# Kernel optimization log

Hardware: AMD Instinct MI355X
Metric: run time of the kernel (lower is better)

Reference implementation:

```python
import jax, jax.numpy as jnp
import numpy as np

E = 16          # num experts
D_IN = 1024     # input_size
D_OUT = 4096    # output_size
TOKENS_PER_EXPERT = 2048
TOTAL_TOKENS = E * TOKENS_PER_EXPERT


def setup_inputs() -> dict:
    key = jax.random.key(0)
    k1, k2 = jax.random.split(key)
    inputs = jax.random.normal(k1, (TOTAL_TOKENS, D_IN), dtype=jnp.float32)
    # init matches nn.init.uniform_(-1/input_size, 1/input_size)
    weight = jax.random.uniform(k2, (E, D_IN, D_OUT), dtype=jnp.float32,
                                minval=-1.0 / D_IN, maxval=1.0 / D_IN)
    # per-expert token counts; host-side numpy constant (like expert_size.tolist() in torch)
    expert_size = np.full((E,), TOKENS_PER_EXPERT, dtype=np.int64)
    return {"inputs": inputs, "expert_size": expert_size, "weight": weight}


def grouped_mm(inputs, weight, sizes):
    # sizes: python ints (static). Each contiguous chunk of tokens hits its expert's weight.
    offs = np.concatenate([[0], np.cumsum(sizes)])
    outs = [inputs[offs[i]:offs[i + 1]] @ weight[i] for i in range(len(sizes))]
    return jnp.concatenate(outs, axis=0)  # [total_tokens, D_OUT]


def reference(inputs, expert_size, weight):
    sizes = np.asarray(expert_size).tolist()  # static split sizes, as in torch.split
    return grouped_mm(inputs, weight, sizes)
```

## Files before the change

### kernel.cpp

```cpp
#include <hip/hip_runtime.h>
#include <hip/hip_bf16.h>


#define E_NUM 16
#define M_PER_E 2048
#define K_DIM 1024
#define N_DIM 4096

#define A_ELEMS (E_NUM * M_PER_E * K_DIM)
#define W_ELEMS (E_NUM * K_DIM * N_DIM)
#define WS_NEEDED ((size_t)A_ELEMS * 2 + (size_t)W_ELEMS * 2)

typedef float  float4v  __attribute__((ext_vector_type(4)));
typedef float  f32x4    __attribute__((ext_vector_type(4)));
typedef short  bf16x8   __attribute__((ext_vector_type(8)));
typedef unsigned short ushort4v __attribute__((ext_vector_type(4)));
typedef unsigned short ushort8v __attribute__((ext_vector_type(8)));

__device__ __forceinline__ ushort4v cvt4_bf16(float4v f) {
    union { __bf16 h[4]; ushort4v u; } x;
#pragma unroll
    for (int j = 0; j < 4; ++j) x.h[j] = (__bf16)f[j];
    return x.u;
}

__global__ __launch_bounds__(256) void convertA_kernel(
    const float* __restrict__ A, unsigned short* __restrict__ out, int n8)
{
    int idx = blockIdx.x * 256 + threadIdx.x;
    int stride = gridDim.x * 256;
    for (int i = idx; i < n8; i += stride) {
        float4v a = *reinterpret_cast<const float4v*>(A + (size_t)i * 8);
        float4v b = *reinterpret_cast<const float4v*>(A + (size_t)i * 8 + 4);
        ushort8v v;
        ushort4v va = cvt4_bf16(a), vb = cvt4_bf16(b);
#pragma unroll
        for (int j = 0; j < 4; ++j) { v[j] = va[j]; v[j + 4] = vb[j]; }
        *reinterpret_cast<ushort8v*>(out + (size_t)i * 8) = v;
    }
}

__global__ __launch_bounds__(256) void transposeW_kernel(
    const float* __restrict__ W, unsigned short* __restrict__ WT)
{
    const int nt = blockIdx.x;
    const int kt = blockIdx.y;
    const int e  = blockIdx.z;
    const int t  = threadIdx.x;

    __shared__ __align__(16) float T[64 * 64];

    const float* Wb = W + ((size_t)e * K_DIM + (size_t)kt * 64) * N_DIM + nt * 64;

#pragma unroll
    for (int j = 0; j < 4; ++j) {
        int kl = (t >> 4) + j * 16;
        int n4 = t & 15;
        float4v v = *reinterpret_cast<const float4v*>(Wb + (size_t)kl * N_DIM + n4 * 4);
        int sp = n4 ^ ((kl >> 3) & 7);
        *reinterpret_cast<float4v*>(&T[kl * 64 + sp * 4]) = v;
    }
    __syncthreads();

#pragma unroll
    for (int c = 0; c < 2; ++c) {
        int nl = (t >> 3) + c * 32;
        int kc = t & 7;
        ushort8v v;
#pragma unroll
        for (int j = 0; j < 8; ++j) {
            int kl = kc * 8 + j;
            int sp = (nl >> 2) ^ kc;
            float f = T[kl * 64 + sp * 4 + (nl & 3)];
            union { __bf16 h; unsigned short u; } cv; cv.h = (__bf16)f;
            v[j] = cv.u;
        }
        unsigned short* dst = WT + ((size_t)e * N_DIM + (size_t)nt * 64 + nl) * K_DIM
                              + (size_t)kt * 64 + kc * 8;
        *reinterpret_cast<ushort8v*>(dst) = v;
    }
}

#define GBM 256
#define GBN 256
#define GBK 64
#define GKT (K_DIM / GBK)

__global__ __launch_bounds__(512, 2) void gemm_bf16_kernel(
    const unsigned short* __restrict__ A,
    const unsigned short* __restrict__ B,
    float* __restrict__ C)
{
    const int bid = blockIdx.x;
    const int swzid = (bid & 7) * (2048 / 8) + (bid >> 3);
    const int e   = swzid >> 7;
    const int rem = swzid & 127;
    const int bm  = rem >> 4;
    const int bn  = rem & 15;

    const int tid  = threadIdx.x;
    const int lane = tid & 63;
    const int wid  = tid >> 6;
    const int wm   = wid >> 2;
    const int wn   = wid & 3;
    const int lrow = lane & 15;
    const int kq   = lane >> 4;

    __shared__ __align__(16) unsigned short sA[2][GBM * GBK];
    __shared__ __align__(16) unsigned short sB[2][GBN * GBK];

    const unsigned short* Abase = A + ((size_t)e * M_PER_E + (size_t)bm * GBM) * K_DIM;
    const unsigned short* Bbase = B + ((size_t)e * N_DIM  + (size_t)bn * GBN) * K_DIM;
    float*                Cbase = C + ((size_t)e * M_PER_E + (size_t)bm * GBM) * N_DIM
                                    + (size_t)bn * GBN;

    const int schunk = (lane & 7) ^ ((lane >> 3) & 7);
    const int srow   = lane >> 3;

    auto STAGE = [&](int p, int kt) {
        const unsigned short* ak = Abase + (size_t)kt * GBK + schunk * 8;
        const unsigned short* bk = Bbase + (size_t)kt * GBK + schunk * 8;
#pragma unroll
        for (int i = 0; i < 4; ++i) {
            const int rb = i * 64 + wid * 8;
            __builtin_amdgcn_global_load_lds(
                (const __attribute__((address_space(1))) void*)(ak + (size_t)(rb + srow) * K_DIM),
                (__attribute__((address_space(3))) void*)&sA[p][rb * GBK], 16, 0, 0);
            __builtin_amdgcn_global_load_lds(
                (const __attribute__((address_space(1))) void*)(bk + (size_t)(rb + srow) * K_DIM),
                (__attribute__((address_space(3))) void*)&sB[p][rb * GBK], 16, 0, 0);
        }
    };

    f32x4 acc[8][4];
#pragma unroll
    for (int mf = 0; mf < 8; ++mf)
#pragma unroll
        for (int nf = 0; nf < 4; ++nf) acc[mf][nf] = (f32x4)0.0f;

    bf16x8 af[8][2], bf[4][2];

    auto READ_ALL = [&](int p) {
#pragma unroll
        for (int s = 0; s < 2; ++s) {
            const int slot = (s * 4 + kq) ^ (lrow & 7);
#pragma unroll
            for (int mf = 0; mf < 4; ++mf) {
                int row = wm * 128 + mf * 16 + lrow;
                af[mf][s] = *reinterpret_cast<const bf16x8*>(&sA[p][row * GBK + slot * 8]);
            }
#pragma unroll
            for (int nf = 0; nf < 4; ++nf) {
                int row = wn * 64 + nf * 16 + lrow;
                bf[nf][s] = *reinterpret_cast<const bf16x8*>(&sB[p][row * GBK + slot * 8]);
            }
        }
#pragma unroll
        for (int s = 0; s < 2; ++s) {
            const int slot = (s * 4 + kq) ^ (lrow & 7);
#pragma unroll
            for (int mf = 4; mf < 8; ++mf) {
                int row = wm * 128 + mf * 16 + lrow;
                af[mf][s] = *reinterpret_cast<const bf16x8*>(&sA[p][row * GBK + slot * 8]);
            }
        }
    };

    auto MMQ = [&](int mh, int nh) {
        __builtin_amdgcn_s_setprio(1);
#pragma unroll
        for (int s = 0; s < 2; ++s)
#pragma unroll
            for (int nf = nh * 2; nf < nh * 2 + 2; ++nf)
#pragma unroll
                for (int mf = mh * 4; mf < mh * 4 + 4; ++mf)
                    acc[mf][nf] = __builtin_amdgcn_mfma_f32_16x16x32_bf16(
                        af[mf][s], bf[nf][s], acc[mf][nf], 0, 0, 0);
        __builtin_amdgcn_s_setprio(0);
    };

    STAGE(0, 0);
    STAGE(1, 1);
    asm volatile("s_waitcnt vmcnt(8)" ::: "memory");
    __builtin_amdgcn_s_barrier();

#pragma unroll 1
    for (int t = 0; t < GKT; ++t) {
        const int p = t & 1;
        READ_ALL(p);
        MMQ(0, 0); MMQ(0, 1);
        asm volatile("s_waitcnt lgkmcnt(0)" ::: "memory");
        __builtin_amdgcn_s_barrier();
        if (t < GKT - 2) STAGE(p, t + 2);
        MMQ(1, 0); MMQ(1, 1);
        if (t < GKT - 1) {
            if (t < GKT - 2)
                asm volatile("s_waitcnt vmcnt(8)" ::: "memory");
            else
                asm volatile("s_waitcnt vmcnt(0)" ::: "memory");
            __builtin_amdgcn_s_barrier();
        }
    }

#pragma unroll
    for (int mf = 0; mf < 8; ++mf) {
#pragma unroll
        for (int nf = 0; nf < 4; ++nf) {
#pragma unroll
            for (int j = 0; j < 4; ++j) {
                int row = wm * 128 + mf * 16 + kq * 4 + j;
                int col = wn * 64 + nf * 16 + lrow;
                Cbase[(size_t)row * N_DIM + col] = acc[mf][nf][j];
            }
        }
    }
}

#define BM 128
#define BN 128
#define BK 64
#define KT (K_DIM / BK)

__device__ __forceinline__ int swz_f(int row, int kelem) {
    return kelem ^ (((row ^ (row >> 3)) & 7) << 3);
}

__global__ __launch_bounds__(256) void grouped_gemm_fused_kernel(
    const float* __restrict__ A, const float* __restrict__ W, float* __restrict__ C)
{
    const int bn = blockIdx.x;
    const int bm = blockIdx.y;
    const int e  = blockIdx.z;
    const int tid  = threadIdx.x;
    const int lane = tid & 63;
    const int wid  = tid >> 6;
    const int wr   = wid >> 1;
    const int wc   = wid & 1;

    __shared__ __align__(16) unsigned short fA[BM * BK];
    __shared__ __align__(16) unsigned short fB[BN * BK];

    const float* Abase = A + ((size_t)e * M_PER_E + (size_t)bm * BM) * K_DIM;
    const float* Wbase = W + (size_t)e * K_DIM * N_DIM + (size_t)bn * BN;
    float*       Cbase = C + ((size_t)e * M_PER_E + (size_t)bm * BM) * N_DIM + (size_t)bn * BN;

    const int arow  = tid >> 4;
    const int acol4 = (tid & 15) * 4;
    const int bkq   = tid >> 4;
    const int bnq   = tid & 15;

    f32x4 acc[4][4];
#pragma unroll
    for (int m = 0; m < 4; ++m)
#pragma unroll
        for (int n = 0; n < 4; ++n) acc[m][n] = (f32x4)0.0f;

    float4v ra[8], rb[8];

    auto LOADT = [&](int kt) {
        const float* ap = Abase + (size_t)arow * K_DIM + kt * BK + acol4;
#pragma unroll
        for (int i = 0; i < 8; ++i)
            ra[i] = *reinterpret_cast<const float4v*>(ap + (size_t)i * 16 * K_DIM);
        const float* bp = Wbase + (size_t)(kt * BK + bkq * 4) * N_DIM + bnq * 4;
#pragma unroll
        for (int i = 0; i < 2; ++i)
#pragma unroll
            for (int r = 0; r < 4; ++r)
                rb[i * 4 + r] = *reinterpret_cast<const float4v*>(bp + (size_t)r * N_DIM + i * 64);
    };

    auto STORET = [&]() {
#pragma unroll
        for (int i = 0; i < 8; ++i) {
            int row = arow + i * 16;
            ushort4v v = cvt4_bf16(ra[i]);
            *reinterpret_cast<ushort4v*>(&fA[row * BK + swz_f(row, acol4)]) = v;
        }
#pragma unroll
        for (int i = 0; i < 2; ++i) {
#pragma unroll
            for (int j = 0; j < 4; ++j) {
                int n = (bnq + i * 16) * 4 + j;
                float4v col;
                col[0] = rb[i * 4 + 0][j];
                col[1] = rb[i * 4 + 1][j];
                col[2] = rb[i * 4 + 2][j];
                col[3] = rb[i * 4 + 3][j];
                ushort4v v = cvt4_bf16(col);
                *reinterpret_cast<ushort4v*>(&fB[n * BK + swz_f(n, bkq * 4)]) = v;
            }
        }
    };

    auto COMPUTE = [&]() {
#pragma unroll
        for (int s = 0; s < 2; ++s) {
            bf16x8 af[4], bfr[4];
            const int ke = s * 32 + (lane >> 4) * 8;
#pragma unroll
            for (int m = 0; m < 4; ++m) {
                int row = wr * 64 + m * 16 + (lane & 15);
                af[m] = *reinterpret_cast<const bf16x8*>(&fA[row * BK + swz_f(row, ke)]);
            }
#pragma unroll
            for (int n = 0; n < 4; ++n) {
                int row = wc * 64 + n * 16 + (lane & 15);
                bfr[n] = *reinterpret_cast<const bf16x8*>(&fB[row * BK + swz_f(row, ke)]);
            }
#pragma unroll
            for (int m = 0; m < 4; ++m)
#pragma unroll
                for (int n = 0; n < 4; ++n)
                    acc[m][n] = __builtin_amdgcn_mfma_f32_16x16x32_bf16(
                        af[m], bfr[n], acc[m][n], 0, 0, 0);
        }
    };

    LOADT(0);
    STORET();
    __syncthreads();
    for (int kt = 0; kt < KT; ++kt) {
        if (kt + 1 < KT) LOADT(kt + 1);
        COMPUTE();
        __syncthreads();
        if (kt + 1 < KT) STORET();
        __syncthreads();
    }

#pragma unroll
    for (int m = 0; m < 4; ++m)
#pragma unroll
        for (int n = 0; n < 4; ++n)
#pragma unroll
            for (int j = 0; j < 4; ++j) {
                int row = wr * 64 + m * 16 + (lane >> 4) * 4 + j;
                int col = wc * 64 + n * 16 + (lane & 15);
                Cbase[(size_t)row * N_DIM + col] = acc[m][n][j];
            }
}

extern "C" void kernel_launch(void* const* d_in, const int* in_sizes, int n_in,
                              void* d_out, int out_size, void* d_ws, size_t ws_size,
                              hipStream_t stream) {
    const float* A = (const float*)d_in[0];
    const float* W = (const float*)d_in[2];
    float* out = (float*)d_out;

    if (ws_size >= WS_NEEDED) {
        unsigned short* wsA = (unsigned short*)d_ws;
        unsigned short* wsW = wsA + (size_t)A_ELEMS;

        hipLaunchKernelGGL(convertA_kernel, dim3(2048), dim3(256), 0, stream,
                           A, wsA, A_ELEMS / 8);
        hipLaunchKernelGGL(transposeW_kernel, dim3(N_DIM / 64, K_DIM / 64, E_NUM),
                           dim3(256), 0, stream, W, wsW);
        hipLaunchKernelGGL(gemm_bf16_kernel, dim3(2048), dim3(512), 0, stream,
                           wsA, wsW, out);
    } else {
        dim3 grid(N_DIM / BN, M_PER_E / BM, E_NUM);
        hipLaunchKernelGGL(grouped_gemm_fused_kernel, grid, dim3(256), 0, stream,
                           A, W, out);
    }
}
```

Before: 470.3 us.

## Interleave half-tile global-to-LDS staging with quarter MFMA phases in GEMM loop

Result: no change. 463.3 us, median of 2 (-1.5%).

```diff
diff --git a/kernel.cpp b/kernel.cpp
--- a/kernel.cpp
+++ b/kernel.cpp
@@ -85,6 +85,9 @@
 #define GBN 256
 #define GBK 64
 #define GKT (K_DIM / GBK)
+
+#define BAR()   __builtin_amdgcn_s_barrier()
+#define LGKM0() asm volatile("s_waitcnt lgkmcnt(0)" ::: "memory")
 
 __global__ __launch_bounds__(512, 2) void gemm_bf16_kernel(
     const unsigned short* __restrict__ A,
@@ -117,18 +120,24 @@
     const int schunk = (lane & 7) ^ ((lane >> 3) & 7);
     const int srow   = lane >> 3;
 
-    auto STAGE = [&](int p, int kt) {
-        const unsigned short* ak = Abase + (size_t)kt * GBK + schunk * 8;
-        const unsigned short* bk = Bbase + (size_t)kt * GBK + schunk * 8;
-#pragma unroll
-        for (int i = 0; i < 4; ++i) {
-            const int rb = i * 64 + wid * 8;
+    auto STAGE_A = [&](int t, int h) {
+        const unsigned short* g = Abase + (size_t)t * GBK + schunk * 8;
+#pragma unroll
+        for (int j = 0; j < 2; ++j) {
+            const int rb = h * 128 + (wid * 2 + j) * 8;
             __builtin_amdgcn_global_load_lds(
-                (const __attribute__((address_space(1))) void*)(ak + (size_t)(rb + srow) * K_DIM),
-                (__attribute__((address_space(3))) void*)&sA[p][rb * GBK], 16, 0, 0);
+                (const __attribute__((address_space(1))) void*)(g + (size_t)(rb + srow) * K_DIM),
+                (__attribute__((address_space(3))) void*)&sA[t & 1][rb * GBK], 16, 0, 0);
+        }
+    };
+    auto STAGE_B = [&](int t, int h) {
+        const unsigned short* g = Bbase + (size_t)t * GBK + schunk * 8;
+#pragma unroll
+        for (int j = 0; j < 2; ++j) {
+            const int rb = h * 128 + (wid * 2 + j) * 8;
             __builtin_amdgcn_global_load_lds(
-                (const __attribute__((address_space(1))) void*)(bk + (size_t)(rb + srow) * K_DIM),
-                (__attribute__((address_space(3))) void*)&sB[p][rb * GBK], 16, 0, 0);
+                (const __attribute__((address_space(1))) void*)(g + (size_t)(rb + srow) * K_DIM),
+                (__attribute__((address_space(3))) void*)&sB[t & 1][rb * GBK], 16, 0, 0);
         }
     };
 
@@ -138,30 +147,28 @@
 #pragma unroll
         for (int nf = 0; nf < 4; ++nf) acc[mf][nf] = (f32x4)0.0f;
 
-    bf16x8 af[8][2], bf[4][2];
-
-    auto READ_ALL = [&](int p) {
+    bf16x8 af[4][2];
+    bf16x8 bf[4][2];
+
+    auto READ_A = [&](int p, int mh) {
 #pragma unroll
         for (int s = 0; s < 2; ++s) {
             const int slot = (s * 4 + kq) ^ (lrow & 7);
 #pragma unroll
             for (int mf = 0; mf < 4; ++mf) {
-                int row = wm * 128 + mf * 16 + lrow;
+                int row = wm * 128 + mh * 64 + mf * 16 + lrow;
                 af[mf][s] = *reinterpret_cast<const bf16x8*>(&sA[p][row * GBK + slot * 8]);
             }
-#pragma unroll
-            for (int nf = 0; nf < 4; ++nf) {
-                int row = wn * 64 + nf * 16 + lrow;
-                bf[nf][s] = *reinterpret_cast<const bf16x8*>(&sB[p][row * GBK + slot * 8]);
-            }
-        }
+        }
+    };
+    auto READ_B = [&](int p, int bh) {
 #pragma unroll
         for (int s = 0; s < 2; ++s) {
             const int slot = (s * 4 + kq) ^ (lrow & 7);
 #pragma unroll
-            for (int mf = 4; mf < 8; ++mf) {
-                int row = wm * 128 + mf * 16 + lrow;
-                af[mf][s] = *reinterpret_cast<const bf16x8*>(&sA[p][row * GBK + slot * 8]);
+            for (int nf = 0; nf < 2; ++nf) {
+                int row = wn * 64 + (bh * 2 + nf) * 16 + lrow;
+                bf[bh * 2 + nf][s] = *reinterpret_cast<const bf16x8*>(&sB[p][row * GBK + slot * 8]);
             }
         }
     };
@@ -173,32 +180,51 @@
 #pragma unroll
             for (int nf = nh * 2; nf < nh * 2 + 2; ++nf)
 #pragma unroll
-                for (int mf = mh * 4; mf < mh * 4 + 4; ++mf)
-                    acc[mf][nf] = __builtin_amdgcn_mfma_f32_16x16x32_bf16(
-                        af[mf][s], bf[nf][s], acc[mf][nf], 0, 0, 0);
+                for (int mf = 0; mf < 4; ++mf)
+                    acc[mh * 4 + mf][nf] = __builtin_amdgcn_mfma_f32_16x16x32_bf16(
+                        af[mf][s], bf[nf][s], acc[mh * 4 + mf][nf], 0, 0, 0);
         __builtin_amdgcn_s_setprio(0);
     };
 
-    STAGE(0, 0);
-    STAGE(1, 1);
-    asm volatile("s_waitcnt vmcnt(8)" ::: "memory");
-    __builtin_amdgcn_s_barrier();
+    STAGE_B(0, 0); STAGE_A(0, 0); STAGE_A(0, 1); STAGE_B(0, 1);
+    STAGE_B(1, 0); STAGE_A(1, 0);
+    asm volatile("s_waitcnt vmcnt(4)" ::: "memory");
+    BAR();
 
 #pragma unroll 1
-    for (int t = 0; t < GKT; ++t) {
-        const int p = t & 1;
-        READ_ALL(p);
-        MMQ(0, 0); MMQ(0, 1);
-        asm volatile("s_waitcnt lgkmcnt(0)" ::: "memory");
-        __builtin_amdgcn_s_barrier();
-        if (t < GKT - 2) STAGE(p, t + 2);
-        MMQ(1, 0); MMQ(1, 1);
-        if (t < GKT - 1) {
-            if (t < GKT - 2)
-                asm volatile("s_waitcnt vmcnt(8)" ::: "memory");
-            else
-                asm volatile("s_waitcnt vmcnt(0)" ::: "memory");
-            __builtin_amdgcn_s_barrier();
+    for (int i = 0; i < GKT / 2; ++i) {
+        const int u = 2 * i;
+        const int v = 2 * i + 1;
+        READ_A(0, 0); READ_B(0, 0);
+        STAGE_A(v, 1);
+        BAR(); LGKM0(); MMQ(0, 0); BAR();
+        READ_B(0, 1);
+        STAGE_B(v, 1);
+        BAR(); LGKM0(); MMQ(0, 1); BAR();
+        READ_A(0, 1);
+        if (u + 2 < GKT) STAGE_B(u + 2, 0);
+        BAR(); LGKM0(); MMQ(1, 0); BAR();
+        if (u + 2 < GKT) STAGE_A(u + 2, 0);
+        BAR(); MMQ(1, 1);
+        if (i < GKT / 2 - 1)
+            asm volatile("s_waitcnt vmcnt(4)" ::: "memory");
+        else
+            asm volatile("s_waitcnt vmcnt(0)" ::: "memory");
+        BAR();
+        READ_A(1, 0); READ_B(1, 0);
+        if (u + 2 < GKT) STAGE_A(u + 2, 1);
+        BAR(); LGKM0(); MMQ(0, 0); BAR();
+        READ_B(1, 1);
+        if (u + 2 < GKT) STAGE_B(u + 2, 1);
+        BAR(); LGKM0(); MMQ(0, 1); BAR();
+        READ_A(1, 1);
+        if (v + 2 < GKT) STAGE_B(v + 2, 0);
+        BAR(); LGKM0(); MMQ(1, 0); BAR();
+        if (v + 2 < GKT) STAGE_A(v + 2, 0);
+        BAR(); MMQ(1, 1);
+        if (i < GKT / 2 - 1) {
+            asm volatile("s_waitcnt vmcnt(4)" ::: "memory");
+            BAR();
         }
     }
 
```
